# Optimization experiments

Hardware: AMD Instinct MI355X
Metric: run time of the kernel (lower is better)

Reference implementation:

```python
import jax, jax.numpy as jnp
import numpy as np

B, S, HID = 2, 2048, 1024
NH, NKV, HD = 16, 4, 64
MAXPOS, THETA, EPS = 4096, 10000.0, 1e-6


def _rope_tables():
    inv_freq = 1.0 / (THETA ** (jnp.arange(0, HD, 2, dtype=jnp.float32) / HD))
    t = jnp.arange(MAXPOS, dtype=jnp.float32)
    freqs = jnp.outer(t, inv_freq)                      # [MAXPOS, HD/2]
    emb = jnp.concatenate([freqs, freqs], axis=-1)      # [MAXPOS, HD]
    return jnp.cos(emb), jnp.sin(emb)


def setup_inputs() -> dict:
    key = jax.random.key(0)
    ks = jax.random.split(key, 8)
    cos, sin = _rope_tables()
    neg = jnp.finfo(jnp.float32).min
    causal = jnp.where(jnp.tril(jnp.ones((S, S), dtype=bool)), 0.0, neg)
    sc = 0.02
    return {
        "hidden_states": jax.random.normal(ks[0], (B, S, HID), jnp.float32),
        "cos": cos,
        "sin": sin,
        "position_ids": jnp.broadcast_to(jnp.arange(S, dtype=jnp.int32), (B, S)),
        "attention_mask": causal[None, None, :, :],
        "Wq": jax.random.normal(ks[1], (NH * HD, HID), jnp.float32) * sc,
        "Wk": jax.random.normal(ks[2], (NKV * HD, HID), jnp.float32) * sc,
        "Wv": jax.random.normal(ks[3], (NKV * HD, HID), jnp.float32) * sc,
        "Wo": jax.random.normal(ks[4], (HID, NH * HD), jnp.float32) * sc,
        "q_norm_w": jnp.ones((HD,), jnp.float32),
        "k_norm_w": jnp.ones((HD,), jnp.float32),
    }


def _rms_norm(x, w):
    xf = x.astype(jnp.float32)
    var = jnp.mean(xf * xf, axis=-1, keepdims=True)
    return (w * (xf * jax.lax.rsqrt(var + EPS))).astype(x.dtype)


def _rotate_half(x):
    x1, x2 = jnp.split(x, 2, axis=-1)
    return jnp.concatenate([-x2, x1], axis=-1)


def reference(hidden_states, cos, sin, position_ids, attention_mask,
              Wq, Wk, Wv, Wo, q_norm_w, k_norm_w):
    b, s, _ = hidden_states.shape
    # projections -> [b, heads, s, hd]
    q = (hidden_states @ Wq.T).reshape(b, s, NH, HD).transpose(0, 2, 1, 3)
    k = (hidden_states @ Wk.T).reshape(b, s, NKV, HD).transpose(0, 2, 1, 3)
    v = (hidden_states @ Wv.T).reshape(b, s, NKV, HD).transpose(0, 2, 1, 3)
    # per-head RMS norm on head_dim
    q = _rms_norm(q, q_norm_w)
    k = _rms_norm(k, k_norm_w)
    # rotary embedding (unsqueeze_dim=1 -> broadcast over heads)
    c = cos[position_ids][:, None, :, :]  # [b,1,s,hd]
    sn = sin[position_ids][:, None, :, :]
    q = q * c + _rotate_half(q) * sn
    k = k * c + _rotate_half(k) * sn
    # GQA: repeat kv heads
    n_rep = NH // NKV
    k = jnp.repeat(k, n_rep, axis=1)
    v = jnp.repeat(v, n_rep, axis=1)
    # attention
    scores = jnp.einsum("bhqd,bhkd->bhqk", q, k) / np.sqrt(HD).astype(np.float32)
    scores = scores + attention_mask
    probs = jax.nn.softmax(scores.astype(jnp.float32), axis=-1).astype(q.dtype)
    ctx = jnp.einsum("bhqk,bhkd->bhqd", probs, v)  # [b,NH,s,hd]
    ctx = ctx.transpose(0, 2, 1, 3).reshape(b, s, NH * HD)
    return ctx @ Wo.T
```

## Files before the change

### kernel.cpp

```cpp
#include <hip/hip_runtime.h>
#include <stdint.h>

#define S_LEN 2048
#define HIDDEN 1024
#define NH 16
#define NKV 4
#define HD 64

typedef unsigned short u16;
typedef __attribute__((ext_vector_type(8))) short short8;
typedef __attribute__((ext_vector_type(4))) float f32x4;
typedef __attribute__((ext_vector_type(16))) float f32x16;
typedef __attribute__((ext_vector_type(4))) uint32_t u32x4;

__device__ __forceinline__ u16 f2b(float f) {
  uint32_t u = __float_as_uint(f);
  uint32_t r = u + 0x7fffu + ((u >> 16) & 1u);
  return (u16)(r >> 16);
}
__device__ __forceinline__ float b2f(u16 b) {
  return __uint_as_float(((uint32_t)b) << 16);
}
__device__ __forceinline__ void gll16(const void* g, void* l) {
  __builtin_amdgcn_global_load_lds(
      (const __attribute__((address_space(1))) uint32_t*)g,
      (__attribute__((address_space(3))) uint32_t*)l, 16, 0, 0);
}

__global__ __launch_bounds__(256) void f2b_kernel(const float* __restrict__ src,
                                                  u16* __restrict__ dst, int n8) {
  int i = blockIdx.x * 256 + threadIdx.x;
  if (i >= n8) return;
  f32x4 a = *reinterpret_cast<const f32x4*>(&src[(size_t)i * 8]);
  f32x4 b = *reinterpret_cast<const f32x4*>(&src[(size_t)i * 8 + 4]);
  short8 t;
#pragma unroll
  for (int k = 0; k < 4; ++k) t[k] = (short)f2b(a[k]);
#pragma unroll
  for (int k = 0; k < 4; ++k) t[4 + k] = (short)f2b(b[k]);
  *reinterpret_cast<short8*>(&dst[(size_t)i * 8]) = t;
}

template <int OUT_BF16>
__global__ __launch_bounds__(256) void gemm_bt(const u16* __restrict__ A,
                                               const u16* __restrict__ B,
                                               void* __restrict__ Cv,
                                               int M, int N, int K) {
  __shared__ u16 As[128][32];
  __shared__ u16 Bs[128][32];
  const int tid = threadIdx.x;
  const int wid = tid >> 6, lane = tid & 63;
  const int fr = lane & 15, fg = lane >> 4;
  const int m0 = blockIdx.x * 128, n0 = blockIdx.y * 128;
  const int wr = wid >> 1, wc = wid & 1;
  const int srow = lane >> 2, scol = (lane & 3) << 3;
  f32x4 acc[4][4] = {};

  for (int k0 = 0; k0 < K; k0 += 32) {
    __syncthreads();
#pragma unroll
    for (int i = 0; i < 2; ++i) {
      const int c = wid + i * 4;
      gll16(&A[(size_t)(m0 + c * 16 + srow) * K + k0 + scol], &As[c * 16][0]);
      gll16(&B[(size_t)(n0 + c * 16 + srow) * K + k0 + scol], &Bs[c * 16][0]);
    }
    __syncthreads();
    short8 a[4], b[4];
#pragma unroll
    for (int i = 0; i < 4; ++i) {
      a[i] = *reinterpret_cast<const short8*>(&As[wr * 64 + i * 16 + fr][fg * 8]);
      b[i] = *reinterpret_cast<const short8*>(&Bs[wc * 64 + i * 16 + fr][fg * 8]);
    }
#pragma unroll
    for (int i = 0; i < 4; ++i)
#pragma unroll
      for (int j = 0; j < 4; ++j)
        acc[i][j] = __builtin_amdgcn_mfma_f32_16x16x32_bf16(a[i], b[j], acc[i][j], 0, 0, 0);
  }

  const int rb = fg * 4;
#pragma unroll
  for (int i = 0; i < 4; ++i)
#pragma unroll
    for (int j = 0; j < 4; ++j) {
      const int row0 = m0 + wr * 64 + i * 16 + rb;
      const int col = n0 + wc * 64 + j * 16 + fr;
#pragma unroll
      for (int r = 0; r < 4; ++r) {
        size_t idx = (size_t)(row0 + r) * N + col;
        if (OUT_BF16) ((u16*)Cv)[idx] = f2b(acc[i][j][r]);
        else          ((float*)Cv)[idx] = acc[i][j][r];
      }
    }
}

__global__ __launch_bounds__(256) void normrope(const u16* __restrict__ qkv,
                                                const int* __restrict__ pos_ids,
                                                const float* __restrict__ cosT,
                                                const float* __restrict__ sinT,
                                                const float* __restrict__ qw,
                                                const float* __restrict__ kw,
                                                u16* __restrict__ Qn,
                                                u16* __restrict__ Kn) {
  const int w = blockIdx.x * 4 + (threadIdx.x >> 6);
  const int lane = threadIdx.x & 63;
  const int row = w / 20, unit = w % 20;
  const int b = row >> 11, s = row & 2047;
  float x = b2f(qkv[(size_t)row * 1536 + unit * 64 + lane]);
  const bool isq = unit < 16;
  const int h = isq ? unit : unit - 16;
  float ss = x * x;
  ss += __shfl_xor(ss, 1);
  ss += __shfl_xor(ss, 2);
  ss += __shfl_xor(ss, 4);
  ss += __shfl_xor(ss, 8);
  ss += __shfl_xor(ss, 16);
  ss += __shfl_xor(ss, 32);
  float r = rsqrtf(ss * (1.0f / 64.0f) + 1e-6f);
  float xn = x * r * (isq ? qw[lane] : kw[lane]);
  const int p = pos_ids[row];
  const float c = cosT[p * 64 + lane];
  const float sn = sinT[p * 64 + lane];
  float partner = __shfl_xor(xn, 32);
  float out = xn * c + (lane < 32 ? -partner : partner) * sn;
  if (isq) Qn[((size_t)(b * NH + h) * S_LEN + s) * HD + lane] = f2b(out);
  else     Kn[((size_t)(b * NKV + h) * S_LEN + s) * HD + lane] = f2b(out);
}

__global__ __launch_bounds__(256) void vtrans(const u16* __restrict__ qkv,
                                              u16* __restrict__ Vt) {
  const int s0 = blockIdx.x * 64;
  const int b = blockIdx.y >> 2, hv = blockIdx.y & 3;
  __shared__ u16 t[64][72];
  const int tid = threadIdx.x;
  const int r = tid >> 2, cq = (tid & 3) << 4;
#pragma unroll
  for (int i = 0; i < 2; ++i)
    *reinterpret_cast<short8*>(&t[r][cq + i * 8]) =
        *reinterpret_cast<const short8*>(
            &qkv[(size_t)(b * S_LEN + s0 + r) * 1536 + 1280 + hv * 64 + cq + i * 8]);
  __syncthreads();
  const int d = tid >> 2, sq = (tid & 3) << 4;
#pragma unroll
  for (int i = 0; i < 2; ++i) {
    u16 tmp[8];
#pragma unroll
    for (int k = 0; k < 8; ++k) tmp[k] = t[sq + i * 8 + k][d];
    *reinterpret_cast<short8*>(
        &Vt[((size_t)(b * NKV + hv) * HD + d) * S_LEN + s0 + sq + i * 8]) =
        *reinterpret_cast<short8*>(tmp);
  }
}

__global__ __launch_bounds__(256) void attn_kernel(const u16* __restrict__ Qn,
                                                   const u16* __restrict__ Kn,
                                                   const u16* __restrict__ Vt,
                                                   u16* __restrict__ ctx) {
  const int bh = blockIdx.y;
  const int b = bh >> 4, h = bh & 15, hkv = h >> 2;
  const u16* Q = Qn + (size_t)bh * S_LEN * HD;
  const u16* K = Kn + (size_t)(b * NKV + hkv) * S_LEN * HD;
  const u16* V = Vt + (size_t)(b * NKV + hkv) * HD * S_LEN;
  const int wid = threadIdx.x >> 6, lane = threadIdx.x & 63;
  const int col = lane & 31, hi = lane >> 5;
  const int j = blockIdx.x;
  int qt;
  if (wid == 0) qt = j;
  else if (wid == 1) qt = 31 - j;
  else if (wid == 2) qt = 32 + j;
  else qt = 63 - j;
  const int q0 = qt * 32;

  short8 qf[4];
#pragma unroll
  for (int d = 0; d < 4; ++d)
    qf[d] = *reinterpret_cast<const short8*>(&Q[(size_t)(q0 + col) * HD + d * 16 + hi * 8]);

  f32x16 o0 = {}, o1 = {};
  float m = -3.0e38f, l = 0.0f;
  const float SC = 0.125f;

  for (int kt = 0; kt <= qt; ++kt) {
    const int kv0 = kt * 32;
    f32x16 s = {};
#pragma unroll
    for (int d = 0; d < 4; ++d) {
      short8 kf = *reinterpret_cast<const short8*>(
          &K[(size_t)(kv0 + col) * HD + d * 16 + hi * 8]);
      s = __builtin_amdgcn_mfma_f32_32x32x16_bf16(kf, qf[d], s, 0, 0, 0);
    }
    if (kt == qt) {
#pragma unroll
      for (int r = 0; r < 16; ++r) {
        int kvr = (r & 3) + 8 * (r >> 2) + 4 * hi;
        s[r] = (kvr <= col) ? s[r] : -3.0e38f;
      }
    }
    float t8[8];
#pragma unroll
    for (int r = 0; r < 8; ++r) t8[r] = fmaxf(s[r], s[r + 8]);
#pragma unroll
    for (int r = 0; r < 4; ++r) t8[r] = fmaxf(t8[r], t8[r + 4]);
    float tm = fmaxf(fmaxf(t8[0], t8[1]), fmaxf(t8[2], t8[3]));
    tm = fmaxf(tm, __shfl_xor(tm, 32));
    if (!__all(tm <= m + 64.0f)) {
      float mn = fmaxf(m, tm);
      float al = __expf((m - mn) * SC);
      m = mn;
      l *= al;
#pragma unroll
      for (int r = 0; r < 16; ++r) { o0[r] *= al; o1[r] *= al; }
    }
    const float mSC = m * SC;
    float p[16];
#pragma unroll
    for (int r = 0; r < 16; ++r) p[r] = __expf(s[r] * SC - mSC);
    float u8[8];
#pragma unroll
    for (int r = 0; r < 8; ++r) u8[r] = p[r] + p[r + 8];
#pragma unroll
    for (int r = 0; r < 4; ++r) u8[r] += u8[r + 4];
    float ps = (u8[0] + u8[1]) + (u8[2] + u8[3]);
    ps += __shfl_xor(ps, 32);
    l += ps;
    uint32_t w[8], x[8];
#pragma unroll
    for (int i = 0; i < 8; ++i) {
      uint32_t wo;
      asm("v_cvt_pk_bf16_f32 %0, %1, %2" : "=v"(wo) : "v"(p[2 * i]), "v"(p[2 * i + 1]));
      w[i] = wo;
    }
#pragma unroll
    for (int i = 0; i < 8; ++i) x[i] = (uint32_t)__shfl_xor((int)w[i], 32);
    u32x4 bw0 = {hi ? x[2] : w[0], hi ? x[3] : w[1], hi ? w[2] : x[0], hi ? w[3] : x[1]};
    u32x4 bw1 = {hi ? x[6] : w[4], hi ? x[7] : w[5], hi ? w[6] : x[4], hi ? w[7] : x[5]};
    short8 B0 = __builtin_bit_cast(short8, bw0);
    short8 B1 = __builtin_bit_cast(short8, bw1);
    short8 vf;
    vf = *reinterpret_cast<const short8*>(&V[(size_t)col * S_LEN + kv0 + hi * 8]);
    o0 = __builtin_amdgcn_mfma_f32_32x32x16_bf16(vf, B0, o0, 0, 0, 0);
    vf = *reinterpret_cast<const short8*>(&V[(size_t)col * S_LEN + kv0 + 16 + hi * 8]);
    o0 = __builtin_amdgcn_mfma_f32_32x32x16_bf16(vf, B1, o0, 0, 0, 0);
    vf = *reinterpret_cast<const short8*>(&V[(size_t)(32 + col) * S_LEN + kv0 + hi * 8]);
    o1 = __builtin_amdgcn_mfma_f32_32x32x16_bf16(vf, B0, o1, 0, 0, 0);
    vf = *reinterpret_cast<const short8*>(&V[(size_t)(32 + col) * S_LEN + kv0 + 16 + hi * 8]);
    o1 = __builtin_amdgcn_mfma_f32_32x32x16_bf16(vf, B1, o1, 0, 0, 0);
  }

  const float invl = 1.0f / l;
  __shared__ __align__(16) u16 Tl[4][32][72];
#pragma unroll
  for (int r = 0; r < 16; ++r) {
    int dl = (r & 3) + 8 * (r >> 2) + 4 * hi;
    Tl[wid][col][dl] = f2b(o0[r] * invl);
    Tl[wid][col][32 + dl] = f2b(o1[r] * invl);
  }
#pragma unroll
  for (int k2 = 0; k2 < 4; ++k2) {
    short8 vv = *reinterpret_cast<const short8*>(&Tl[wid][col][hi * 32 + k2 * 8]);
    *reinterpret_cast<short8*>(
        &ctx[((size_t)(b * S_LEN) + q0 + col) * (NH * HD) + h * HD + hi * 32 + k2 * 8]) = vv;
  }
}

extern "C" void kernel_launch(void* const* d_in, const int* in_sizes, int n_in,
                              void* d_out, int out_size, void* d_ws, size_t ws_size,
                              hipStream_t stream) {
  const float* hidden = (const float*)d_in[0];
  const float* cosT   = (const float*)d_in[1];
  const float* sinT   = (const float*)d_in[2];
  const int*   pos    = (const int*)d_in[3];
  const float* Wq = (const float*)d_in[5];
  const float* Wk = (const float*)d_in[6];
  const float* Wv = (const float*)d_in[7];
  const float* Wo = (const float*)d_in[8];
  const float* qw = (const float*)d_in[9];
  const float* kw = (const float*)d_in[10];

  char* p = (char*)d_ws;
  u16* hb   = (u16*)p; p += (size_t)4096 * 1024 * 2;
  u16* wqkv = (u16*)p; p += (size_t)1536 * 1024 * 2;
  u16* wob  = (u16*)p; p += (size_t)1024 * 1024 * 2;
  u16* qkvr = (u16*)p; p += (size_t)4096 * 1536 * 2;
  u16* qn   = (u16*)p; p += (size_t)(NH * 2) * S_LEN * HD * 2;
  u16* kn   = (u16*)p; p += (size_t)(NKV * 2) * S_LEN * HD * 2;
  u16* vt   = (u16*)p; p += (size_t)(NKV * 2) * HD * S_LEN * 2;
  u16* ctx  = (u16*)p; p += (size_t)4096 * 1024 * 2;

  f2b_kernel<<<4194304 / 2048, 256, 0, stream>>>(hidden, hb, 4194304 / 8);
  f2b_kernel<<<1048576 / 2048, 256, 0, stream>>>(Wq, wqkv, 1048576 / 8);
  f2b_kernel<<<262144 / 2048, 256, 0, stream>>>(Wk, wqkv + 1048576, 262144 / 8);
  f2b_kernel<<<262144 / 2048, 256, 0, stream>>>(Wv, wqkv + 1310720, 262144 / 8);
  f2b_kernel<<<1048576 / 2048, 256, 0, stream>>>(Wo, wob, 1048576 / 8);

  gemm_bt<1><<<dim3(32, 12), 256, 0, stream>>>(hb, wqkv, qkvr, 4096, 1536, 1024);

  normrope<<<20480, 256, 0, stream>>>(qkvr, pos, cosT, sinT, qw, kw, qn, kn);
  vtrans<<<dim3(32, 8), 256, 0, stream>>>(qkvr, vt);

  attn_kernel<<<dim3(16, 2 * NH), 256, 0, stream>>>(qn, kn, vt, ctx);

  gemm_bt<0><<<dim3(32, 8), 256, 0, stream>>>(ctx, wob, d_out, 4096, 1024, 1024);
}
```

Measured before the change: 256.6 us.

## Split KV range across warps per query tile and fold softmax scale into Q

After: 281.8 us. 9.8% more time.

```diff
diff --git a/kernel.cpp b/kernel.cpp
--- a/kernel.cpp
+++ b/kernel.cpp
@@ -117,7 +117,7 @@
   ss += __shfl_xor(ss, 16);
   ss += __shfl_xor(ss, 32);
   float r = rsqrtf(ss * (1.0f / 64.0f) + 1e-6f);
-  float xn = x * r * (isq ? qw[lane] : kw[lane]);
+  float xn = x * r * (isq ? qw[lane] * 0.18033688011112042f : kw[lane]);
   const int p = pos_ids[row];
   const float c = cosT[p * 64 + lane];
   const float sn = sinT[p * 64 + lane];
@@ -163,13 +163,11 @@
   const u16* V = Vt + (size_t)(b * NKV + hkv) * HD * S_LEN;
   const int wid = threadIdx.x >> 6, lane = threadIdx.x & 63;
   const int col = lane & 31, hi = lane >> 5;
-  const int j = blockIdx.x;
-  int qt;
-  if (wid == 0) qt = j;
-  else if (wid == 1) qt = 31 - j;
-  else if (wid == 2) qt = 32 + j;
-  else qt = 63 - j;
+  const int qt = 63 - blockIdx.x;
   const int q0 = qt * 32;
+
+  __shared__ float Om[4][32][65];
+  __shared__ float Ml[4][32], Ll[4][32];
 
   short8 qf[4];
 #pragma unroll
@@ -178,9 +176,8 @@
 
   f32x16 o0 = {}, o1 = {};
   float m = -3.0e38f, l = 0.0f;
-  const float SC = 0.125f;
-
-  for (int kt = 0; kt <= qt; ++kt) {
+
+  for (int kt = wid; kt <= qt; kt += 4) {
     const int kv0 = kt * 32;
     f32x16 s = {};
 #pragma unroll
@@ -203,18 +200,17 @@
     for (int r = 0; r < 4; ++r) t8[r] = fmaxf(t8[r], t8[r + 4]);
     float tm = fmaxf(fmaxf(t8[0], t8[1]), fmaxf(t8[2], t8[3]));
     tm = fmaxf(tm, __shfl_xor(tm, 32));
-    if (!__all(tm <= m + 64.0f)) {
+    if (!__all(tm <= m + 8.0f)) {
       float mn = fmaxf(m, tm);
-      float al = __expf((m - mn) * SC);
+      float al = exp2f(m - mn);
       m = mn;
       l *= al;
 #pragma unroll
       for (int r = 0; r < 16; ++r) { o0[r] *= al; o1[r] *= al; }
     }
-    const float mSC = m * SC;
     float p[16];
 #pragma unroll
-    for (int r = 0; r < 16; ++r) p[r] = __expf(s[r] * SC - mSC);
+    for (int r = 0; r < 16; ++r) p[r] = exp2f(s[r] - m);
     float u8[8];
 #pragma unroll
     for (int r = 0; r < 8; ++r) u8[r] = p[r] + p[r + 8];
@@ -247,20 +243,33 @@
     o1 = __builtin_amdgcn_mfma_f32_32x32x16_bf16(vf, B1, o1, 0, 0, 0);
   }
 
-  const float invl = 1.0f / l;
-  __shared__ __align__(16) u16 Tl[4][32][72];
+  if (hi == 0) { Ml[wid][col] = m; Ll[wid][col] = l; }
 #pragma unroll
   for (int r = 0; r < 16; ++r) {
     int dl = (r & 3) + 8 * (r >> 2) + 4 * hi;
-    Tl[wid][col][dl] = f2b(o0[r] * invl);
-    Tl[wid][col][32 + dl] = f2b(o1[r] * invl);
-  }
-#pragma unroll
-  for (int k2 = 0; k2 < 4; ++k2) {
-    short8 vv = *reinterpret_cast<const short8*>(&Tl[wid][col][hi * 32 + k2 * 8]);
-    *reinterpret_cast<short8*>(
-        &ctx[((size_t)(b * S_LEN) + q0 + col) * (NH * HD) + h * HD + hi * 32 + k2 * 8]) = vv;
-  }
+    Om[wid][col][dl] = o0[r];
+    Om[wid][col][32 + dl] = o1[r];
+  }
+  __syncthreads();
+
+  const int t = threadIdx.x;
+  const int q = t >> 3, d0 = (t & 7) * 8;
+  float M = fmaxf(fmaxf(Ml[0][q], Ml[1][q]), fmaxf(Ml[2][q], Ml[3][q]));
+  float L = 0.0f;
+  float acc[8] = {};
+#pragma unroll
+  for (int w = 0; w < 4; ++w) {
+    float ww = exp2f(Ml[w][q] - M);
+    L += ww * Ll[w][q];
+#pragma unroll
+    for (int k = 0; k < 8; ++k) acc[k] += ww * Om[w][q][d0 + k];
+  }
+  float invL = 1.0f / L;
+  short8 outv;
+#pragma unroll
+  for (int k = 0; k < 8; ++k) outv[k] = (short)f2b(acc[k] * invL);
+  *reinterpret_cast<short8*>(
+      &ctx[((size_t)(b * S_LEN) + q0 + q) * (NH * HD) + h * HD + d0]) = outv;
 }
 
 extern "C" void kernel_launch(void* const* d_in, const int* in_sizes, int n_in,
@@ -298,7 +307,7 @@
   normrope<<<20480, 256, 0, stream>>>(qkvr, pos, cosT, sinT, qw, kw, qn, kn);
   vtrans<<<dim3(32, 8), 256, 0, stream>>>(qkvr, vt);
 
-  attn_kernel<<<dim3(16, 2 * NH), 256, 0, stream>>>(qn, kn, vt, ctx);
+  attn_kernel<<<dim3(64, 2 * NH), 256, 0, stream>>>(qn, kn, vt, ctx);
 
   gemm_bt<0><<<dim3(32, 8), 256, 0, stream>>>(ctx, wob, d_out, 4096, 1024, 1024);
 }
```

## Split attention into two independent softmax streams, fold scale into Q, merge casts

Applied to the files above, without the earlier changes.

Result: faster. 251.0 us (-2.2%).

```diff
diff --git a/kernel.cpp b/kernel.cpp
--- a/kernel.cpp
+++ b/kernel.cpp
@@ -27,18 +27,30 @@
       (__attribute__((address_space(3))) uint32_t*)l, 16, 0, 0);
 }
 
-__global__ __launch_bounds__(256) void f2b_kernel(const float* __restrict__ src,
-                                                  u16* __restrict__ dst, int n8) {
+__global__ __launch_bounds__(256) void f2b_multi(
+    const float* __restrict__ s0, u16* __restrict__ d0, int n0,
+    const float* __restrict__ s1, u16* __restrict__ d1, int n1,
+    const float* __restrict__ s2, u16* __restrict__ d2, int n2,
+    const float* __restrict__ s3, u16* __restrict__ d3, int n3,
+    const float* __restrict__ s4, u16* __restrict__ d4, int n4) {
   int i = blockIdx.x * 256 + threadIdx.x;
-  if (i >= n8) return;
-  f32x4 a = *reinterpret_cast<const f32x4*>(&src[(size_t)i * 8]);
-  f32x4 b = *reinterpret_cast<const f32x4*>(&src[(size_t)i * 8 + 4]);
+  const float* s;
+  u16* d;
+  int idx = i;
+  if (i < n0) { s = s0; d = d0; }
+  else if ((idx = i - n0) < n1) { s = s1; d = d1; }
+  else if ((idx = i - n0 - n1) < n2) { s = s2; d = d2; }
+  else if ((idx = i - n0 - n1 - n2) < n3) { s = s3; d = d3; }
+  else if ((idx = i - n0 - n1 - n2 - n3) < n4) { s = s4; d = d4; }
+  else return;
+  f32x4 a = *reinterpret_cast<const f32x4*>(&s[(size_t)idx * 8]);
+  f32x4 b = *reinterpret_cast<const f32x4*>(&s[(size_t)idx * 8 + 4]);
   short8 t;
 #pragma unroll
   for (int k = 0; k < 4; ++k) t[k] = (short)f2b(a[k]);
 #pragma unroll
   for (int k = 0; k < 4; ++k) t[4 + k] = (short)f2b(b[k]);
-  *reinterpret_cast<short8*>(&dst[(size_t)i * 8]) = t;
+  *reinterpret_cast<short8*>(&d[(size_t)idx * 8]) = t;
 }
 
 template <int OUT_BF16>
@@ -117,7 +129,7 @@
   ss += __shfl_xor(ss, 16);
   ss += __shfl_xor(ss, 32);
   float r = rsqrtf(ss * (1.0f / 64.0f) + 1e-6f);
-  float xn = x * r * (isq ? qw[lane] : kw[lane]);
+  float xn = x * r * (isq ? qw[lane] * 0.18033688011112042f : kw[lane]);
   const int p = pos_ids[row];
   const float c = cosT[p * 64 + lane];
   const float sn = sinT[p * 64 + lane];
@@ -150,6 +162,74 @@
         &Vt[((size_t)(b * NKV + hv) * HD + d) * S_LEN + s0 + sq + i * 8]) =
         *reinterpret_cast<short8*>(tmp);
   }
+}
+
+__device__ __forceinline__ void attn_tile(const u16* __restrict__ K,
+                                          const u16* __restrict__ V,
+                                          const short8 qf[4], int kv0, bool domask,
+                                          int col, int hi,
+                                          f32x16& o0, f32x16& o1, float& m, float& l) {
+  short8 v0 = *reinterpret_cast<const short8*>(&V[(size_t)col * S_LEN + kv0 + hi * 8]);
+  short8 v1 = *reinterpret_cast<const short8*>(&V[(size_t)col * S_LEN + kv0 + 16 + hi * 8]);
+  short8 v2 = *reinterpret_cast<const short8*>(&V[(size_t)(32 + col) * S_LEN + kv0 + hi * 8]);
+  short8 v3 = *reinterpret_cast<const short8*>(&V[(size_t)(32 + col) * S_LEN + kv0 + 16 + hi * 8]);
+  f32x16 s = {};
+#pragma unroll
+  for (int d = 0; d < 4; ++d) {
+    short8 kf = *reinterpret_cast<const short8*>(
+        &K[(size_t)(kv0 + col) * HD + d * 16 + hi * 8]);
+    s = __builtin_amdgcn_mfma_f32_32x32x16_bf16(kf, qf[d], s, 0, 0, 0);
+  }
+  if (domask) {
+#pragma unroll
+    for (int r = 0; r < 16; ++r) {
+      int kvr = (r & 3) + 8 * (r >> 2) + 4 * hi;
+      s[r] = (kvr <= col) ? s[r] : -3.0e38f;
+    }
+  }
+  float t8[8];
+#pragma unroll
+  for (int r = 0; r < 8; ++r) t8[r] = fmaxf(s[r], s[r + 8]);
+#pragma unroll
+  for (int r = 0; r < 4; ++r) t8[r] = fmaxf(t8[r], t8[r + 4]);
+  float tm = fmaxf(fmaxf(t8[0], t8[1]), fmaxf(t8[2], t8[3]));
+  tm = fmaxf(tm, __shfl_xor(tm, 32));
+  if (!__all(tm <= m + 8.0f)) {
+    float mn = fmaxf(m, tm);
+    float al = exp2f(m - mn);
+    m = mn;
+    l *= al;
+#pragma unroll
+    for (int r = 0; r < 16; ++r) { o0[r] *= al; o1[r] *= al; }
+  }
+  float p[16];
+#pragma unroll
+  for (int r = 0; r < 16; ++r) p[r] = exp2f(s[r] - m);
+  float u8[8];
+#pragma unroll
+  for (int r = 0; r < 8; ++r) u8[r] = p[r] + p[r + 8];
+#pragma unroll
+  for (int r = 0; r < 4; ++r) u8[r] += u8[r + 4];
+  float ps = (u8[0] + u8[1]) + (u8[2] + u8[3]);
+  ps += __shfl_xor(ps, 32);
+  l += ps;
+  uint32_t w[8], x[8];
+#pragma unroll
+  for (int i = 0; i < 8; ++i) {
+    uint32_t wo;
+    asm("v_cvt_pk_bf16_f32 %0, %1, %2" : "=v"(wo) : "v"(p[2 * i]), "v"(p[2 * i + 1]));
+    w[i] = wo;
+  }
+#pragma unroll
+  for (int i = 0; i < 8; ++i) x[i] = (uint32_t)__shfl_xor((int)w[i], 32);
+  u32x4 bw0 = {hi ? x[2] : w[0], hi ? x[3] : w[1], hi ? w[2] : x[0], hi ? w[3] : x[1]};
+  u32x4 bw1 = {hi ? x[6] : w[4], hi ? x[7] : w[5], hi ? w[6] : x[4], hi ? w[7] : x[5]};
+  short8 B0 = __builtin_bit_cast(short8, bw0);
+  short8 B1 = __builtin_bit_cast(short8, bw1);
+  o0 = __builtin_amdgcn_mfma_f32_32x32x16_bf16(v0, B0, o0, 0, 0, 0);
+  o0 = __builtin_amdgcn_mfma_f32_32x32x16_bf16(v1, B1, o0, 0, 0, 0);
+  o1 = __builtin_amdgcn_mfma_f32_32x32x16_bf16(v2, B0, o1, 0, 0, 0);
+  o1 = __builtin_amdgcn_mfma_f32_32x32x16_bf16(v3, B1, o1, 0, 0, 0);
 }
 
 __global__ __launch_bounds__(256) void attn_kernel(const u16* __restrict__ Qn,
@@ -176,84 +256,27 @@
   for (int d = 0; d < 4; ++d)
     qf[d] = *reinterpret_cast<const short8*>(&Q[(size_t)(q0 + col) * HD + d * 16 + hi * 8]);
 
-  f32x16 o0 = {}, o1 = {};
-  float m = -3.0e38f, l = 0.0f;
-  const float SC = 0.125f;
-
-  for (int kt = 0; kt <= qt; ++kt) {
-    const int kv0 = kt * 32;
-    f32x16 s = {};
-#pragma unroll
-    for (int d = 0; d < 4; ++d) {
-      short8 kf = *reinterpret_cast<const short8*>(
-          &K[(size_t)(kv0 + col) * HD + d * 16 + hi * 8]);
-      s = __builtin_amdgcn_mfma_f32_32x32x16_bf16(kf, qf[d], s, 0, 0, 0);
-    }
-    if (kt == qt) {
-#pragma unroll
-      for (int r = 0; r < 16; ++r) {
-        int kvr = (r & 3) + 8 * (r >> 2) + 4 * hi;
-        s[r] = (kvr <= col) ? s[r] : -3.0e38f;
-      }
-    }
-    float t8[8];
-#pragma unroll
-    for (int r = 0; r < 8; ++r) t8[r] = fmaxf(s[r], s[r + 8]);
-#pragma unroll
-    for (int r = 0; r < 4; ++r) t8[r] = fmaxf(t8[r], t8[r + 4]);
-    float tm = fmaxf(fmaxf(t8[0], t8[1]), fmaxf(t8[2], t8[3]));
-    tm = fmaxf(tm, __shfl_xor(tm, 32));
-    if (!__all(tm <= m + 64.0f)) {
-      float mn = fmaxf(m, tm);
-      float al = __expf((m - mn) * SC);
-      m = mn;
-      l *= al;
-#pragma unroll
-      for (int r = 0; r < 16; ++r) { o0[r] *= al; o1[r] *= al; }
-    }
-    const float mSC = m * SC;
-    float p[16];
-#pragma unroll
-    for (int r = 0; r < 16; ++r) p[r] = __expf(s[r] * SC - mSC);
-    float u8[8];
-#pragma unroll
-    for (int r = 0; r < 8; ++r) u8[r] = p[r] + p[r + 8];
-#pragma unroll
-    for (int r = 0; r < 4; ++r) u8[r] += u8[r + 4];
-    float ps = (u8[0] + u8[1]) + (u8[2] + u8[3]);
-    ps += __shfl_xor(ps, 32);
-    l += ps;
-    uint32_t w[8], x[8];
-#pragma unroll
-    for (int i = 0; i < 8; ++i) {
-      uint32_t wo;
-      asm("v_cvt_pk_bf16_f32 %0, %1, %2" : "=v"(wo) : "v"(p[2 * i]), "v"(p[2 * i + 1]));
-      w[i] = wo;
-    }
-#pragma unroll
-    for (int i = 0; i < 8; ++i) x[i] = (uint32_t)__shfl_xor((int)w[i], 32);
-    u32x4 bw0 = {hi ? x[2] : w[0], hi ? x[3] : w[1], hi ? w[2] : x[0], hi ? w[3] : x[1]};
-    u32x4 bw1 = {hi ? x[6] : w[4], hi ? x[7] : w[5], hi ? w[6] : x[4], hi ? w[7] : x[5]};
-    short8 B0 = __builtin_bit_cast(short8, bw0);
-    short8 B1 = __builtin_bit_cast(short8, bw1);
-    short8 vf;
-    vf = *reinterpret_cast<const short8*>(&V[(size_t)col * S_LEN + kv0 + hi * 8]);
-    o0 = __builtin_amdgcn_mfma_f32_32x32x16_bf16(vf, B0, o0, 0, 0, 0);
-    vf = *reinterpret_cast<const short8*>(&V[(size_t)col * S_LEN + kv0 + 16 + hi * 8]);
-    o0 = __builtin_amdgcn_mfma_f32_32x32x16_bf16(vf, B1, o0, 0, 0, 0);
-    vf = *reinterpret_cast<const short8*>(&V[(size_t)(32 + col) * S_LEN + kv0 + hi * 8]);
-    o1 = __builtin_amdgcn_mfma_f32_32x32x16_bf16(vf, B0, o1, 0, 0, 0);
-    vf = *reinterpret_cast<const short8*>(&V[(size_t)(32 + col) * S_LEN + kv0 + 16 + hi * 8]);
-    o1 = __builtin_amdgcn_mfma_f32_32x32x16_bf16(vf, B1, o1, 0, 0, 0);
-  }
-
+  f32x16 oA0 = {}, oA1 = {}, oB0 = {}, oB1 = {};
+  float mA = -3.0e38f, lA = 0.0f, mB = -3.0e38f, lB = 0.0f;
+
+  int kt = 0;
+  for (; kt + 1 <= qt; kt += 2) {
+    attn_tile(K, V, qf, kt * 32, false, col, hi, oA0, oA1, mA, lA);
+    attn_tile(K, V, qf, (kt + 1) * 32, kt + 1 == qt, col, hi, oB0, oB1, mB, lB);
+  }
+  if (kt <= qt)
+    attn_tile(K, V, qf, kt * 32, kt == qt, col, hi, oA0, oA1, mA, lA);
+
+  float M = fmaxf(mA, mB);
+  float wA = exp2f(mA - M), wB = exp2f(mB - M);
+  float l = wA * lA + wB * lB;
   const float invl = 1.0f / l;
   __shared__ __align__(16) u16 Tl[4][32][72];
 #pragma unroll
   for (int r = 0; r < 16; ++r) {
     int dl = (r & 3) + 8 * (r >> 2) + 4 * hi;
-    Tl[wid][col][dl] = f2b(o0[r] * invl);
-    Tl[wid][col][32 + dl] = f2b(o1[r] * invl);
+    Tl[wid][col][dl] = f2b((wA * oA0[r] + wB * oB0[r]) * invl);
+    Tl[wid][col][32 + dl] = f2b((wA * oA1[r] + wB * oB1[r]) * invl);
   }
 #pragma unroll
   for (int k2 = 0; k2 < 4; ++k2) {
@@ -287,11 +310,11 @@
   u16* vt   = (u16*)p; p += (size_t)(NKV * 2) * HD * S_LEN * 2;
   u16* ctx  = (u16*)p; p += (size_t)4096 * 1024 * 2;
 
-  f2b_kernel<<<4194304 / 2048, 256, 0, stream>>>(hidden, hb, 4194304 / 8);
-  f2b_kernel<<<1048576 / 2048, 256, 0, stream>>>(Wq, wqkv, 1048576 / 8);
-  f2b_kernel<<<262144 / 2048, 256, 0, stream>>>(Wk, wqkv + 1048576, 262144 / 8);
-  f2b_kernel<<<262144 / 2048, 256, 0, stream>>>(Wv, wqkv + 1310720, 262144 / 8);
-  f2b_kernel<<<1048576 / 2048, 256, 0, stream>>>(Wo, wob, 1048576 / 8);
+  f2b_multi<<<3332, 256, 0, stream>>>(hidden, hb, 524288,
+                                      Wq, wqkv, 131072,
+                                      Wk, wqkv + 1048576, 32768,
+                                      Wv, wqkv + 1310720, 32768,
+                                      Wo, wob, 131072);
 
   gemm_bt<1><<<dim3(32, 12), 256, 0, stream>>>(hb, wqkv, qkvr, 4096, 1536, 1024);
 
```
